# Kernel tuning notes

Hardware: AMD Instinct MI355X
Metric: run time of the kernel (lower is better)

The kernel has to match this reference:

```python
import jax, jax.numpy as jnp
import numpy as np

OUT_H, OUT_W = 512, 512  # output_size init kwarg


def setup_inputs() -> dict:
    key = jax.random.key(0)
    k1, k2, k3 = jax.random.split(key, 3)
    X = jax.random.normal(k1, (16, 512, 512, 16), dtype=jnp.float32)
    scale = jax.random.uniform(k2, (16, 1), dtype=jnp.float32)
    translate = jax.random.normal(k3, (16, 2), dtype=jnp.float32)
    return {"X": X, "scale": scale, "translate": translate}


def reference(X, scale, translate):
    B, H, W, C = X.shape
    # build per-batch 2x3 affine: [[s, 0, tx], [0, s, ty]]
    s = scale[:, 0]
    z = jnp.zeros_like(s)
    theta = jnp.stack([s, z, translate[:, 0], z, s, translate[:, 1]], axis=1).reshape(B, 2, 3)

    # regular grid in [-1, 1], homogeneous coords: [3, N], N = OUT_H*OUT_W
    x_lin = jnp.linspace(-1.0, 1.0, OUT_W)
    y_lin = jnp.linspace(-1.0, 1.0, OUT_H)
    xc, yc = jnp.meshgrid(x_lin, y_lin)  # each [OUT_H, OUT_W], 'xy' indexing as in tf.meshgrid
    grid = jnp.stack([xc.ravel(), yc.ravel(), jnp.ones(OUT_H * OUT_W, dtype=jnp.float32)], axis=0)

    # sampled grid: [B, 2, N]
    sg = jnp.einsum('bij,jn->bin', theta, grid)
    # map from [-1,1] to pixel coords; original multiplies by W (not W-1) -- keep faithful
    x = 0.5 * (sg[:, 0, :] + 1.0) * W  # [B, N]
    y = 0.5 * (sg[:, 1, :] + 1.0) * H

    # corner indices: TF cast truncates toward zero, as does astype(int32)
    x0 = x.astype(jnp.int32)
    x1 = x0 + 1
    y0 = y.astype(jnp.int32)
    y1 = y0 + 1
    x0 = jnp.clip(x0, 0, W - 1)
    x1 = jnp.clip(x1, 0, W - 1)
    y0 = jnp.clip(y0, 0, H - 1)
    y1 = jnp.clip(y1, 0, H - 1)

    # gather 4 neighbors: [B, N, C]
    b = jnp.arange(B)[:, None]
    pa = X[b, y0, x0]
    pb = X[b, y1, x0]
    pc = X[b, y0, x1]
    pd = X[b, y1, x1]

    # bilinear weights use the clipped integer corners recast to float (as original)
    x0f = x0.astype(x.dtype)
    x1f = x1.astype(x.dtype)
    y0f = y0.astype(y.dtype)
    y1f = y1.astype(y.dtype)
    wa = ((x1f - x) * (y1f - y))[..., None]
    wb = ((x1f - x) * (y - y0f))[..., None]
    wc = ((x - x0f) * (y1f - y))[..., None]
    wd = ((x - x0f) * (y - y0f))[..., None]

    out = wa * pa + wb * pb + wc * pc + wd * pd  # [B, N, C]
    return out.reshape(B, OUT_H, OUT_W, C)
```

## Files before the change

### kernel.cpp

```cpp
#include <hip/hip_runtime.h>


#define BH   512
#define BW   512
#define BC   16
#define NB   16

__global__ __launch_bounds__(256) void bilerp_kernel(
    const float* __restrict__ X,
    const float* __restrict__ scale,
    const float* __restrict__ translate,
    float* __restrict__ out)
{
    const int blk = blockIdx.x;
    const int b  = blk >> 9;
    const int i  = blk & 511;

    const float s  = scale[b];
    const float tx = translate[2 * b];
    const float ty = translate[2 * b + 1];

    const float yl = -1.0f + 2.0f * (float)i / 511.0f;
    const float y  = 0.5f * (s * yl + ty + 1.0f) * (float)BH;
    int y0 = (int)y;
    int y1 = y0 + 1;
    y0 = min(max(y0, 0), BH - 1);
    y1 = min(max(y1, 0), BH - 1);
    const float wy1 = (float)y1 - y;
    const float wy0 = y - (float)y0;

    const float4* __restrict__ Xb   = (const float4*)(X + (size_t)b * BH * BW * BC);
    const float4* __restrict__ row0 = Xb + (size_t)y0 * (BW * (BC / 4));
    const float4* __restrict__ row1 = Xb + (size_t)y1 * (BW * (BC / 4));
    float4* __restrict__ orow = (float4*)(out + (size_t)blk * BW * BC);

    const int tid = threadIdx.x;
    const int q   = tid & 3;
    const int p0  = tid >> 2;

    #pragma unroll
    for (int j = p0; j < BW; j += 64) {
        const float xl = -1.0f + 2.0f * (float)j / 511.0f;
        const float x  = 0.5f * (s * xl + tx + 1.0f) * (float)BW;
        int x0 = (int)x;
        int x1 = x0 + 1;
        x0 = min(max(x0, 0), BW - 1);
        x1 = min(max(x1, 0), BW - 1);
        const float wx1 = (float)x1 - x;
        const float wx0 = x - (float)x0;

        const float wa = wx1 * wy1;
        const float wb = wx1 * wy0;
        const float wc = wx0 * wy1;
        const float wd = wx0 * wy0;

        const float4 pa = row0[x0 * 4 + q];
        const float4 pb = row1[x0 * 4 + q];
        const float4 pc = row0[x1 * 4 + q];
        const float4 pd = row1[x1 * 4 + q];

        float4 o;
        o.x = wa * pa.x + wb * pb.x + wc * pc.x + wd * pd.x;
        o.y = wa * pa.y + wb * pb.y + wc * pc.y + wd * pd.y;
        o.z = wa * pa.z + wb * pb.z + wc * pc.z + wd * pd.z;
        o.w = wa * pa.w + wb * pb.w + wc * pc.w + wd * pd.w;

        orow[j * 4 + q] = o;
    }
}

extern "C" void kernel_launch(void* const* d_in, const int* in_sizes, int n_in,
                              void* d_out, int out_size, void* d_ws, size_t ws_size,
                              hipStream_t stream) {
    const float* X         = (const float*)d_in[0];
    const float* scale     = (const float*)d_in[1];
    const float* translate = (const float*)d_in[2];
    float* out             = (float*)d_out;

    dim3 grid(NB * BH);
    dim3 block(256);
    bilerp_kernel<<<grid, block, 0, stream>>>(X, scale, translate, out);
}
```

Measured before the change: 409.5 us.

## Remap blocks to XCDs for L2 locality and use nontemporal output stores

Block IDs are remapped so that each of the 8 XCDs, which receive blocks round-robin, handles a contiguous range of 1024 output rows. Adjacent rows of the same batch then share input rows in that XCD's L2 instead of being spread across all XCDs. Output stores become nontemporal so the streamed output does not evict reused input lines, and the math moves to ext_vector_type arithmetic. The mapping assumes exactly 8 XCDs with round-robin dispatch and a grid of 8192 blocks.

```diff
diff --git a/kernel.cpp b/kernel.cpp
--- a/kernel.cpp
+++ b/kernel.cpp
@@ -6,15 +6,20 @@
 #define BC   16
 #define NB   16
 
+typedef float floatx4 __attribute__((ext_vector_type(4)));
+
 __global__ __launch_bounds__(256) void bilerp_kernel(
     const float* __restrict__ X,
     const float* __restrict__ scale,
     const float* __restrict__ translate,
     float* __restrict__ out)
 {
-    const int blk = blockIdx.x;
-    const int b  = blk >> 9;
-    const int i  = blk & 511;
+    const int bid  = blockIdx.x;
+    const int xcd  = bid & 7;
+    const int slot = bid >> 3;
+    const int w    = xcd * 1024 + slot;
+    const int b  = w >> 9;
+    const int i  = w & 511;
 
     const float s  = scale[b];
     const float tx = translate[2 * b];
@@ -29,10 +34,10 @@
     const float wy1 = (float)y1 - y;
     const float wy0 = y - (float)y0;
 
-    const float4* __restrict__ Xb   = (const float4*)(X + (size_t)b * BH * BW * BC);
-    const float4* __restrict__ row0 = Xb + (size_t)y0 * (BW * (BC / 4));
-    const float4* __restrict__ row1 = Xb + (size_t)y1 * (BW * (BC / 4));
-    float4* __restrict__ orow = (float4*)(out + (size_t)blk * BW * BC);
+    const floatx4* __restrict__ Xb   = (const floatx4*)(X + (size_t)b * BH * BW * BC);
+    const floatx4* __restrict__ row0 = Xb + (size_t)y0 * (BW * (BC / 4));
+    const floatx4* __restrict__ row1 = Xb + (size_t)y1 * (BW * (BC / 4));
+    floatx4* __restrict__ orow = (floatx4*)(out + (size_t)w * BW * BC);
 
     const int tid = threadIdx.x;
     const int q   = tid & 3;
@@ -54,18 +59,14 @@
         const float wc = wx0 * wy1;
         const float wd = wx0 * wy0;
 
-        const float4 pa = row0[x0 * 4 + q];
-        const float4 pb = row1[x0 * 4 + q];
-        const float4 pc = row0[x1 * 4 + q];
-        const float4 pd = row1[x1 * 4 + q];
+        const floatx4 pa = row0[x0 * 4 + q];
+        const floatx4 pb = row1[x0 * 4 + q];
+        const floatx4 pc = row0[x1 * 4 + q];
+        const floatx4 pd = row1[x1 * 4 + q];
 
-        float4 o;
-        o.x = wa * pa.x + wb * pb.x + wc * pc.x + wd * pd.x;
-        o.y = wa * pa.y + wb * pb.y + wc * pc.y + wd * pd.y;
-        o.z = wa * pa.z + wb * pb.z + wc * pc.z + wd * pd.z;
-        o.w = wa * pa.w + wb * pb.w + wc * pc.w + wd * pd.w;
+        const floatx4 o = wa * pa + wb * pb + wc * pc + wd * pd;
 
-        orow[j * 4 + q] = o;
+        __builtin_nontemporal_store(o, &orow[j * 4 + q]);
     }
 }
 
```

Result: slower. 426.5 us (+4.2%).
